# Performance work log

Measured on AMD Instinct MI355X. Metric: run time of the kernel, lower is better.

## Reference

```python
import jax, jax.numpy as jnp
import numpy as np

B, L, N, F = 8, 4096, 128, 128          # batch, pixels (64x64), memories, filters
H, DK, DV = 8, 16, 32                   # heads, key dim/head, value dim/head
TK, TV = H * DK, H * DV                 # total key depth 128, total value depth 256
BOT, FFN = 256, 2048                    # bottleneck (2*filters), feed-forward channels
EPS = 1e-3                              # keras BatchNormalization epsilon
INV = float(1.0 / np.sqrt(1.0 + EPS))   # inference BN with moving mean=0, var=1


def _bn_pair(k, shape):
    kg, kb = jax.random.split(k)
    gamma = jax.random.uniform(kg, shape, jnp.float32, 0.5, 1.5)
    beta = 0.1 * jax.random.normal(kb, shape, jnp.float32)
    return jnp.stack([gamma, beta])


def setup_inputs() -> dict:
    key = jax.random.key(0)
    ks = jax.random.split(key, 24)
    s = float(BOT) ** -0.5  # TruncatedNormal(stddev=bottleneck**-0.5) init for qkv convs
    return {
        "pixel_input": jax.random.normal(ks[0], (B, L, F), jnp.float32),
        "memory_input": jax.random.normal(ks[1], (B, N, F), jnp.float32),
        "W_mem1": 0.05 * jax.random.normal(ks[2], (F, BOT), jnp.float32),
        "bn_mem1": _bn_pair(ks[3], (BOT,)),
        "W_pix1": 0.05 * jax.random.normal(ks[4], (F, BOT), jnp.float32),
        "bn_pix1": _bn_pair(ks[5], (BOT,)),
        "W_mem_qkv": s * jax.random.normal(ks[6], (BOT, 2 * TK + TV), jnp.float32),
        "bn_mem_qkv": _bn_pair(ks[7], (2 * TK + TV,)),
        "W_pix_qkv": s * jax.random.normal(ks[8], (BOT, 2 * TK + TV), jnp.float32),
        "bn_pix_qkv": _bn_pair(ks[9], (2 * TK + TV,)),
        "bn_mem_sim": _bn_pair(ks[10], (H,)),
        "bn_mem_ret": _bn_pair(ks[11], (H, DV)),
        "bn_pix_sim": _bn_pair(ks[12], (H,)),
        "bn_pix_ret": _bn_pair(ks[13], (H, DV)),
        "W_mem3": 0.05 * jax.random.normal(ks[14], (TV, F), jnp.float32),
        "bn_mem3": _bn_pair(ks[15], (F,)),
        "W_pix3": 0.05 * jax.random.normal(ks[16], (TV, F), jnp.float32),
        "bn_pix3": _bn_pair(ks[17], (F,)),
        "W_ffn1": 0.05 * jax.random.normal(ks[18], (F, FFN), jnp.float32),
        "bn_ffn1": _bn_pair(ks[19], (FFN,)),
        "W_ffn2": 0.05 * jax.random.normal(ks[20], (FFN, F), jnp.float32),
        "bn_ffn2": _bn_pair(ks[21], (F,)),
    }


def _cbn(x, W, p, relu=False):
    """Conv1D (kernel=1) + inference BatchNorm over channels (+ optional relu)."""
    y = jnp.einsum('blc,cd->bld', x, W)
    y = y * (p[0] * INV) + p[1]
    return jax.nn.relu(y) if relu else y


def _heads(t, d):
    b, l, _ = t.shape  # [b, l, H*d] -> [b, H, l, d]
    return t.reshape(b, l, H, d).transpose(0, 2, 1, 3)


def reference(pixel_input, memory_input, W_mem1, bn_mem1, W_pix1, bn_pix1,
              W_mem_qkv, bn_mem_qkv, W_pix_qkv, bn_pix_qkv,
              bn_mem_sim, bn_mem_ret, bn_pix_sim, bn_pix_ret,
              W_mem3, bn_mem3, W_pix3, bn_pix3,
              W_ffn1, bn_ffn1, W_ffn2, bn_ffn2):
    # Bottleneck projections (conv1 + BN + relu)
    mem = _cbn(memory_input, W_mem1, bn_mem1, True)   # [B, N, BOT]
    pix = _cbn(pixel_input, W_pix1, bn_pix1, True)    # [B, L, BOT]

    # QKV projections (conv + BN, no activation)
    mqkv = _cbn(mem, W_mem_qkv, bn_mem_qkv)           # [B, N, 2*TK+TV]
    pqkv = _cbn(pix, W_pix_qkv, bn_pix_qkv)           # [B, L, 2*TK+TV]
    mq, mk, mv = mqkv[..., :TK], mqkv[..., TK:2 * TK], mqkv[..., 2 * TK:]
    pq, pk, pv = pqkv[..., :TK], pqkv[..., TK:2 * TK], pqkv[..., 2 * TK:]
    mq_h, mk_h = _heads(mq, DK), _heads(mk, DK)       # [B, H, N, DK]
    pq_h, pk_h = _heads(pq, DK), _heads(pk, DK)       # [B, H, L, DK]
    mv_h = mv.reshape(B, N, H, DV)                    # [B, N, H, DV]
    pv_h = pv.reshape(B, L, H, DV)                    # [B, L, H, DV]

    # Memory path: memory2pixel attention + memory self-attention share softmax
    k_cat = jnp.concatenate([pk_h, mk_h], axis=2)     # [B, H, L+N, DK]
    v_cat = jnp.concatenate([pv_h, mv_h], axis=1)     # [B, L+N, H, DV]
    logits = jnp.einsum('bhnd,bhmd->bhnm', mq_h, k_cat)
    logits = logits * (bn_mem_sim[0] * INV)[None, :, None, None] + bn_mem_sim[1][None, :, None, None]
    attn = jax.nn.softmax(logits, axis=-1)
    ret = jnp.einsum('bhnm,bmhd->bhnd', attn, v_cat)  # [B, H, N, DV]
    ret = ret * (bn_mem_ret[0] * INV)[None, :, None, :] + bn_mem_ret[1][None, :, None, :]
    ret = jax.nn.relu(ret).transpose(0, 2, 1, 3).reshape(B, N, TV)
    mem_out = jax.nn.relu(memory_input + _cbn(ret, W_mem3, bn_mem3))
    ffn = _cbn(mem_out, W_ffn1, bn_ffn1, True)
    mem_out = jax.nn.relu(mem_out + _cbn(ffn, W_ffn2, bn_ffn2))

    # Pixel path: pixel2memory feedback attention (sigmoid activation)
    plogits = jnp.einsum('bhld,bhnd->bhln', pq_h, mk_h)
    plogits = plogits * (bn_pix_sim[0] * INV)[None, :, None, None] + bn_pix_sim[1][None, :, None, None]
    pattn = jax.nn.sigmoid(plogits)
    pret = jnp.einsum('bhln,bnhd->bhld', pattn, mv_h)  # [B, H, L, DV]
    pret = pret * (bn_pix_ret[0] * INV)[None, :, None, :] + bn_pix_ret[1][None, :, None, :]
    pret = jax.nn.relu(pret).transpose(0, 2, 1, 3).reshape(B, L, TV)
    pix_out = jax.nn.relu(pixel_input + _cbn(pret, W_pix3, bn_pix3))

    return pix_out, mem_out
```

## Files before the change

kernel.cpp:

```cpp
#include <hip/hip_runtime.h>

typedef __attribute__((ext_vector_type(8))) short short8;
typedef __attribute__((ext_vector_type(4))) float floatx4;

#define INVC 0.9995003746877732f
#define NCHUNK 33

__device__ __forceinline__ unsigned short f2bf(float f) {
    union { float f; unsigned int u; } c; c.f = f;
    unsigned int r = c.u + 0x7fffu + ((c.u >> 16) & 1u);
    return (unsigned short)(r >> 16);
}
__device__ __forceinline__ unsigned int f2bf2(float a, float b) {
    return (unsigned int)f2bf(a) | ((unsigned int)f2bf(b) << 16);
}
__device__ __forceinline__ unsigned long long pack4(float v0, float v1, float v2, float v3) {
    return (unsigned long long)f2bf2(v0, v1) | ((unsigned long long)f2bf2(v2, v3) << 32);
}
__device__ __forceinline__ float bf2f(unsigned short u) {
    union { unsigned int u; float f; } c; c.u = ((unsigned int)u) << 16;
    return c.f;
}
__device__ __forceinline__ void gld_lds16(const unsigned short* g, unsigned short* l) {
    __builtin_amdgcn_global_load_lds(
        (const __attribute__((address_space(1))) unsigned int*)g,
        (__attribute__((address_space(3))) unsigned int*)l, 16, 0, 0);
}
__device__ __forceinline__ int fidx(int row, int k) {
    return (k >> 5) * 512 + (row + 16 * ((k >> 3) & 3)) * 8 + (k & 7);
}

struct PrepPtrs {
    const float* src_pix;
    unsigned short* dst_pix;
    const float* W[8]; unsigned short* Wt[8];
};

__global__ __launch_bounds__(256) void prep_kernel(PrepPtrs P) {
    __shared__ float T[32][33];
    const int bid = blockIdx.x, t = threadIdx.x;
    if (bid < 4096) {
        int i = bid * 1024 + t * 4;
        float4 v = *(const float4*)(P.src_pix + i);
        unsigned long long pk = pack4(v.x, v.y, v.z, v.w);
        *(unsigned long long*)(P.dst_pix + i) = pk;
        return;
    }
    int rel = bid - 4096;
    const int KD[8]  = {128,128,256,256,256,256,128,2048};
    const int ND[8]  = {256,256,512,512,128,128,2048,128};
    const int CNT[8] = {32,32,128,128,32,32,256,256};
    int wi = 0;
    #pragma unroll
    for (int k = 0; k < 8; ++k) { if (rel >= CNT[k] && wi == k) { rel -= CNT[k]; wi = k + 1; } }
    const int K = KD[wi], N = ND[wi];
    const int ntn = N >> 5;
    const int tn = rel % ntn, tk = rel / ntn;
    const int n0 = tn * 32, k0 = tk * 32;
    const float* W = P.W[wi];
    unsigned short* Wt = P.Wt[wi];
    const int tx = t & 31, ty = t >> 5;
    #pragma unroll
    for (int i = 0; i < 4; ++i)
        T[ty + 8*i][tx] = W[(size_t)(k0 + ty + 8*i) * N + n0 + tx];
    __syncthreads();
    #pragma unroll
    for (int i = 0; i < 4; ++i)
        Wt[(size_t)(n0 + ty + 8*i) * K + k0 + tx] = f2bf(T[tx][ty + 8*i]);
}

__device__ __forceinline__ void gemm_body(
    const unsigned short* __restrict__ A,
    const unsigned short* __restrict__ Bt,
    const float* __restrict__ bnp,
    const float* __restrict__ residF,
    float* __restrict__ outF,
    int K, int Nc, int row0, int col0,
    unsigned short* As, unsigned short* Bs)
{
    const int t = threadIdx.x;
    const int lane = t & 63, w = t >> 6;
    const int l15 = lane & 15, quad = lane >> 4;
    const int wr = w >> 1, wc = w & 1;

    floatx4 acc[4][4];
    #pragma unroll
    for (int i = 0; i < 4; ++i)
        #pragma unroll
        for (int j = 0; j < 4; ++j) acc[i][j] = (floatx4){0.f, 0.f, 0.f, 0.f};

    const unsigned short* gA0 = A  + (size_t)(row0 + w*16     + l15) * K + quad*8;
    const unsigned short* gA1 = A  + (size_t)(row0 + (w+4)*16 + l15) * K + quad*8;
    const unsigned short* gB0 = Bt + (size_t)(col0 + w*16     + l15) * K + quad*8;
    const unsigned short* gB1 = Bt + (size_t)(col0 + (w+4)*16 + l15) * K + quad*8;
    unsigned short* lA0 = &As[w * 512];
    unsigned short* lA1 = &As[(w + 4) * 512];
    unsigned short* lB0 = &Bs[w * 512];
    unsigned short* lB1 = &Bs[(w + 4) * 512];

    for (int k0 = 0; k0 < K; k0 += 32) {
        __syncthreads();
        gld_lds16(gA0 + k0, lA0);
        gld_lds16(gA1 + k0, lA1);
        gld_lds16(gB0 + k0, lB0);
        gld_lds16(gB1 + k0, lB1);
        __syncthreads();
        short8 a[4], b[4];
        #pragma unroll
        for (int mt = 0; mt < 4; ++mt) a[mt] = *(const short8*)&As[(wr*4 + mt)*512 + lane*8];
        #pragma unroll
        for (int nt = 0; nt < 4; ++nt) b[nt] = *(const short8*)&Bs[(wc*4 + nt)*512 + lane*8];
        #pragma unroll
        for (int mt = 0; mt < 4; ++mt)
            #pragma unroll
            for (int nt = 0; nt < 4; ++nt)
                acc[mt][nt] = __builtin_amdgcn_mfma_f32_16x16x32_bf16(a[mt], b[nt], acc[mt][nt], 0, 0, 0);
    }

    #pragma unroll
    for (int mt = 0; mt < 4; ++mt) {
        const int rowb = row0 + wr*64 + mt*16 + quad*4;
        #pragma unroll
        for (int nt = 0; nt < 4; ++nt) {
            const int col = col0 + wc*64 + nt*16 + l15;
            floatx4 v = acc[mt][nt];
            const float g  = bnp[col] * INVC;
            const float be = bnp[Nc + col];
            #pragma unroll
            for (int r = 0; r < 4; ++r) {
                size_t off = (size_t)(rowb + r) * Nc + col;
                float v1 = v[r] * g + be + residF[off];
                outF[off] = fmaxf(v1, 0.f);
            }
        }
    }
}

__global__ __launch_bounds__(256, 3) void k_qkv(
    const unsigned short* __restrict__ pixB,
    const unsigned short* __restrict__ Wt1, const float* __restrict__ bn1,
    const unsigned short* __restrict__ Wt2, const float* __restrict__ bnq,
    unsigned short* __restrict__ qip, unsigned short* __restrict__ kip,
    unsigned short* __restrict__ vtp,
    const float* __restrict__ memory_input,
    const unsigned short* __restrict__ Wm0, const float* __restrict__ bnm1,
    const unsigned short* __restrict__ Wm2, const float* __restrict__ bnmq,
    unsigned short* __restrict__ qim, unsigned short* __restrict__ kim,
    unsigned short* __restrict__ vtm)
{
    __shared__ unsigned short A2[32*512];
    const int t = threadIdx.x;
    const int lane = t & 63, w = t >> 6;
    const int l15 = lane & 15, quad = lane >> 4;

    if (blockIdx.x < 512) {
        const int row0 = blockIdx.x * 64;
        const int bb = row0 >> 12;
        const int runit0 = row0 >> 4;
        {
            short8 afr[4][4];
            float ga[4][4], ba[4][4];
            #pragma unroll
            for (int i = 0; i < 4; ++i) {
                #pragma unroll
                for (int kc = 0; kc < 4; ++kc)
                    afr[i][kc] = *(const short8*)&Wt1[(size_t)(w*64 + i*16 + l15)*128 + kc*32 + quad*8];
                #pragma unroll
                for (int r = 0; r < 4; ++r) {
                    const int col = w*64 + i*16 + quad*4 + r;
                    ga[i][r] = bn1[col] * INVC;
                    ba[i][r] = bn1[256 + col];
                }
            }
            #pragma unroll
            for (int ru = 0; ru < 4; ++ru) {
                short8 bfr[4];
                #pragma unroll
                for (int kc = 0; kc < 4; ++kc)
                    bfr[kc] = *(const short8*)&pixB[(size_t)(row0 + ru*16 + l15)*128 + kc*32 + quad*8];
                #pragma unroll
                for (int i = 0; i < 4; ++i) {
                    floatx4 acc = {0.f,0.f,0.f,0.f};
                    #pragma unroll
                    for (int kc = 0; kc < 4; ++kc)
                        acc = __builtin_amdgcn_mfma_f32_16x16x32_bf16(afr[i][kc], bfr[kc], acc, 0, 0, 0);
                    float v[4];
                    #pragma unroll
                    for (int r = 0; r < 4; ++r)
                        v[r] = fmaxf(acc[r]*ga[i][r] + ba[i][r], 0.f);
                    const int unit = ru*8 + w*2 + (i >> 1);
                    const int koff = (i & 1)*2 + (quad >> 1);
                    const int off  = unit*512 + (l15 + 16*koff)*8 + (quad & 1)*4;
                    uint2 pk; pk.x = f2bf2(v[0], v[1]); pk.y = f2bf2(v[2], v[3]);
                    *(uint2*)&A2[off] = pk;
                }
            }
        }
        __syncthreads();

        if (w < 2) {
            const int sec = w * 128;
            unsigned short* img = (w == 0) ? qip : kip;
            const int soff = (l15 + 16*(quad>>1))*8 + (quad&1)*4;
            for (int op = 0; op < 4; ++op) {
                short8 a0[8], a1[8];
                float g2[2][4], be2[2][4];
                #pragma unroll
                for (int kc = 0; kc < 8; ++kc) {
                    a0[kc] = *(const short8*)&Wt2[(size_t)(sec + (op*2+0)*16 + l15)*256 + kc*32 + quad*8];
                    a1[kc] = *(const short8*)&Wt2[(size_t)(sec + (op*2+1)*16 + l15)*256 + kc*32 + quad*8];
                }
                #pragma unroll
                for (int e = 0; e < 2; ++e)
                    #pragma unroll
                    for (int r = 0; r < 4; ++r) {
                        const int col = sec + (op*2+e)*16 + quad*4 + r;
                        g2[e][r] = bnq[col]*INVC; be2[e][r] = bnq[512+col];
                    }
                #pragma unroll
                for (int ru = 0; ru < 4; ++ru) {
                    short8 bv[8];
                    #pragma unroll
                    for (int kc = 0; kc < 8; ++kc)
                        bv[kc] = *(const short8*)&A2[(ru*8+kc)*512 + lane*8];
                    floatx4 acc0 = {0.f,0.f,0.f,0.f}, acc1 = {0.f,0.f,0.f,0.f};
                    #pragma unroll
                    for (int kc = 0; kc < 8; ++kc) {
                        acc0 = __builtin_amdgcn_mfma_f32_16x16x32_bf16(a0[kc], bv[kc], acc0, 0, 0, 0);
                        acc1 = __builtin_amdgcn_mfma_f32_16x16x32_bf16(a1[kc], bv[kc], acc1, 0, 0, 0);
                    }
                    unsigned long long pk0 = pack4(acc0[0]*g2[0][0]+be2[0][0], acc0[1]*g2[0][1]+be2[0][1],
                                                  acc0[2]*g2[0][2]+be2[0][2], acc0[3]*g2[0][3]+be2[0][3]);
                    unsigned long long pk1 = pack4(acc1[0]*g2[1][0]+be2[1][0], acc1[1]*g2[1][1]+be2[1][1],
                                                  acc1[2]*g2[1][2]+be2[1][2], acc1[3]*g2[1][3]+be2[1][3]);
                    *(unsigned long long*)&img[(size_t)((runit0+ru)*8 + op*2+0)*256 + soff] = pk0;
                    *(unsigned long long*)&img[(size_t)((runit0+ru)*8 + op*2+1)*256 + soff] = pk1;
                }
            }
        } else {
            const int dvb = (w-2)*128;
            for (int op = 0; op < 4; ++op) {
                short8 b0[8], b1[8];
                const int dvg0 = dvb + (op*2+0)*16 + l15;
                const int dvg1 = dvb + (op*2+1)*16 + l15;
                #pragma unroll
                for (int kc = 0; kc < 8; ++kc) {
                    b0[kc] = *(const short8*)&Wt2[(size_t)(256 + dvg0)*256 + kc*32 + quad*8];
                    b1[kc] = *(const short8*)&Wt2[(size_t)(256 + dvg1)*256 + kc*32 + quad*8];
                }
                const float gv0 = bnq[256 + dvg0]*INVC, bv0 = bnq[512 + 256 + dvg0];
                const float gv1 = bnq[256 + dvg1]*INVC, bv1 = bnq[512 + 256 + dvg1];
                const int h0 = dvg0 >> 5, dv16_0 = dvg0 & 15, du0 = (dvg0 >> 4) & 1;
                const int h1 = dvg1 >> 5, dv16_1 = dvg1 & 15, du1 = (dvg1 >> 4) & 1;
                #pragma unroll
                for (int ru = 0; ru < 4; ++ru) {
                    short8 av[8];
                    #pragma unroll
                    for (int kc = 0; kc < 8; ++kc)
                        av[kc] = *(const short8*)&A2[(ru*8+kc)*512 + lane*8];
                    floatx4 acc0 = {0.f,0.f,0.f,0.f}, acc1 = {0.f,0.f,0.f,0.f};
                    #pragma unroll
                    for (int kc = 0; kc < 8; ++kc) {
                        acc0 = __builtin_amdgcn_mfma_f32_16x16x32_bf16(av[kc], b0[kc], acc0, 0, 0, 0);
                        acc1 = __builtin_amdgcn_mfma_f32_16x16x32_bf16(av[kc], b1[kc], acc1, 0, 0, 0);
                    }
                    const int keyb = (row0 & 4095) + ru*16 + quad*4;
                    const int kcv = keyb >> 5;
                    const int g3 = (keyb >> 3) & 3;
                    const int jb = (quad & 1)*4;
                    unsigned long long pk0 = pack4(acc0[0]*gv0+bv0, acc0[1]*gv0+bv0,
                                                  acc0[2]*gv0+bv0, acc0[3]*gv0+bv0);
                    unsigned long long pk1 = pack4(acc1[0]*gv1+bv1, acc1[1]*gv1+bv1,
                                                  acc1[2]*gv1+bv1, acc1[3]*gv1+bv1);
                    size_t u0 = (size_t)((bb*8 + h0)*256 + (kcv>>2)*8 + du0*4 + (kcv&3))*512
                              + (dv16_0 + 16*g3)*8 + jb;
                    size_t u1 = (size_t)((bb*8 + h1)*256 + (kcv>>2)*8 + du1*4 + (kcv&3))*512
                              + (dv16_1 + 16*g3)*8 + jb;
                    *(unsigned long long*)&vtp[u0] = pk0;
                    *(unsigned long long*)&vtp[u1] = pk1;
                }
            }
        }
        return;
    }

    unsigned short* A0 = &A2[0];
    unsigned short* A1 = &A2[4*512];
    const int g0 = (blockIdx.x - 512) * 16;
    const int bb = g0 >> 7, ru = (g0 >> 4) & 7;
    {
        const int row = t >> 4;
        const int c0 = (t & 15) * 8;
        const float* src = memory_input + (size_t)(g0 + row) * 128 + c0;
        float4 v0 = *(const float4*)src;
        float4 v1 = *(const float4*)(src + 4);
        float vv[8] = {v0.x, v0.y, v0.z, v0.w, v1.x, v1.y, v1.z, v1.w};
        #pragma unroll
        for (int e = 0; e < 8; ++e)
            A0[fidx(row, c0 + e)] = f2bf(vv[e]);
    }
    __syncthreads();
    #pragma unroll
    for (int i = 0; i < 4; ++i) {
        const int n0 = (w*4 + i) * 16;
        floatx4 acc = {0.f,0.f,0.f,0.f};
        #pragma unroll
        for (int kc = 0; kc < 4; ++kc) {
            short8 a = *(const short8*)&A0[kc*512 + lane*8];
            short8 bfr = *(const short8*)&Wm0[(size_t)(n0 + l15)*128 + kc*32 + quad*8];
            acc = __builtin_amdgcn_mfma_f32_16x16x32_bf16(a, bfr, acc, 0, 0, 0);
        }
        const int col = n0 + l15;
        const float g = bnm1[col] * INVC, be = bnm1[256 + col];
        #pragma unroll
        for (int r = 0; r < 4; ++r)
            A1[fidx(quad*4 + r, col)] = f2bf(fmaxf(acc[r]*g + be, 0.f));
    }
    __syncthreads();
    if (w < 2) {
        const int sec = w * 128;
        unsigned short* img = (w == 0) ? qim : kim;
        const int soff = (l15 + 16*(quad>>1))*8 + (quad&1)*4;
        for (int op = 0; op < 4; ++op) {
            short8 a0[8], a1f[8];
            float g2[2][4], be2[2][4];
            #pragma unroll
            for (int kc = 0; kc < 8; ++kc) {
                a0[kc]  = *(const short8*)&Wm2[(size_t)(sec + (op*2+0)*16 + l15)*256 + kc*32 + quad*8];
                a1f[kc] = *(const short8*)&Wm2[(size_t)(sec + (op*2+1)*16 + l15)*256 + kc*32 + quad*8];
            }
            #pragma unroll
            for (int e = 0; e < 2; ++e)
                #pragma unroll
                for (int r = 0; r < 4; ++r) {
                    const int col = sec + (op*2+e)*16 + quad*4 + r;
                    g2[e][r] = bnmq[col]*INVC; be2[e][r] = bnmq[512+col];
                }
            short8 bv[8];
            #pragma unroll
            for (int kc = 0; kc < 8; ++kc)
                bv[kc] = *(const short8*)&A1[kc*512 + lane*8];
            floatx4 acc0 = {0.f,0.f,0.f,0.f}, acc1 = {0.f,0.f,0.f,0.f};
            #pragma unroll
            for (int kc = 0; kc < 8; ++kc) {
                acc0 = __builtin_amdgcn_mfma_f32_16x16x32_bf16(a0[kc],  bv[kc], acc0, 0, 0, 0);
                acc1 = __builtin_amdgcn_mfma_f32_16x16x32_bf16(a1f[kc], bv[kc], acc1, 0, 0, 0);
            }
            unsigned long long pk0 = pack4(acc0[0]*g2[0][0]+be2[0][0], acc0[1]*g2[0][1]+be2[0][1],
                                          acc0[2]*g2[0][2]+be2[0][2], acc0[3]*g2[0][3]+be2[0][3]);
            unsigned long long pk1 = pack4(acc1[0]*g2[1][0]+be2[1][0], acc1[1]*g2[1][1]+be2[1][1],
                                          acc1[2]*g2[1][2]+be2[1][2], acc1[3]*g2[1][3]+be2[1][3]);
            *(unsigned long long*)&img[(size_t)((bb*8+ru)*8 + op*2+0)*256 + soff] = pk0;
            *(unsigned long long*)&img[(size_t)((bb*8+ru)*8 + op*2+1)*256 + soff] = pk1;
        }
    } else {
        const int dvb = (w-2)*128;
        for (int op = 0; op < 4; ++op) {
            short8 b0[8], b1[8];
            const int dvg0 = dvb + (op*2+0)*16 + l15;
            const int dvg1 = dvb + (op*2+1)*16 + l15;
            #pragma unroll
            for (int kc = 0; kc < 8; ++kc) {
                b0[kc] = *(const short8*)&Wm2[(size_t)(256 + dvg0)*256 + kc*32 + quad*8];
                b1[kc] = *(const short8*)&Wm2[(size_t)(256 + dvg1)*256 + kc*32 + quad*8];
            }
            const float gv0 = bnmq[256 + dvg0]*INVC, bv0 = bnmq[512 + 256 + dvg0];
            const float gv1 = bnmq[256 + dvg1]*INVC, bv1 = bnmq[512 + 256 + dvg1];
            const int h0 = dvg0 >> 5, dv16_0 = dvg0 & 15, du0 = (dvg0 >> 4) & 1;
            const int h1 = dvg1 >> 5, dv16_1 = dvg1 & 15, du1 = (dvg1 >> 4) & 1;
            short8 av[8];
            #pragma unroll
            for (int kc = 0; kc < 8; ++kc)
                av[kc] = *(const short8*)&A1[kc*512 + lane*8];
            floatx4 acc0 = {0.f,0.f,0.f,0.f}, acc1 = {0.f,0.f,0.f,0.f};
            #pragma unroll
            for (int kc = 0; kc < 8; ++kc) {
                acc0 = __builtin_amdgcn_mfma_f32_16x16x32_bf16(av[kc], b0[kc], acc0, 0, 0, 0);
                acc1 = __builtin_amdgcn_mfma_f32_16x16x32_bf16(av[kc], b1[kc], acc1, 0, 0, 0);
            }
            const int keyb = (g0 & 127) + quad*4;
            const int kcv = keyb >> 5;
            const int g3 = (keyb >> 3) & 3;
            const int jb = (quad & 1)*4;
            unsigned long long pk0 = pack4(acc0[0]*gv0+bv0, acc0[1]*gv0+bv0,
                                          acc0[2]*gv0+bv0, acc0[3]*gv0+bv0);
            unsigned long long pk1 = pack4(acc1[0]*gv1+bv1, acc1[1]*gv1+bv1,
                                          acc1[2]*gv1+bv1, acc1[3]*gv1+bv1);
            size_t u0 = (size_t)((bb*8 + h0)*8 + du0*4 + kcv)*512 + (dv16_0 + 16*g3)*8 + jb;
            size_t u1 = (size_t)((bb*8 + h1)*8 + du1*4 + kcv)*512 + (dv16_1 + 16*g3)*8 + jb;
            *(unsigned long long*)&vtm[u0] = pk0;
            *(unsigned long long*)&vtm[u1] = pk1;
        }
    }
}

__global__ __launch_bounds__(256, 4) void k_attn(
    const unsigned short* __restrict__ qip, const unsigned short* __restrict__ kip,
    const unsigned short* __restrict__ vtp,
    const unsigned short* __restrict__ qim, const unsigned short* __restrict__ kim,
    const unsigned short* __restrict__ vtm,
    const float* __restrict__ bn_psim, const float* __restrict__ bn_pret,
    unsigned short* __restrict__ pret,
    const float* __restrict__ bn_msim,
    float* __restrict__ part_acc, float* __restrict__ part_ml)
{
    __shared__ unsigned short Qs[4*512];
    __shared__ unsigned short Ks[8*512];
    __shared__ unsigned short VsT[8*512];
    __shared__ unsigned short Ps[16*512];
    const int t = threadIdx.x;
    const int lane = t & 63, w = t >> 6;
    const int l15 = lane & 15, quad = lane >> 4;
    floatx4 z4 = {0.f, 0.f, 0.f, 0.f};

    const int is_pix = (blockIdx.x < 4096);
    int b, h, qrow0, c = 0, qh = 0;
    const unsigned short *qsrc, *ksrc0, *ksrc1, *vsrc0, *vsrc1;
    if (is_pix) {
        const int bx = blockIdx.x;
        const int lt = bx & 63; h = (bx >> 6) & 7; b = bx >> 9;
        qrow0 = b*4096 + lt*64;
        qsrc  = qip + (size_t)((b*256 + lt*4 + w)*8 + h)*256;
        ksrc0 = kim + (size_t)((b*8 + w)*8 + h)*256;
        ksrc1 = kim + (size_t)((b*8 + w+4)*8 + h)*256;
        vsrc0 = vtm + (size_t)((b*8+h)*8 + w)*512;
        vsrc1 = vtm + (size_t)((b*8+h)*8 + w+4)*512;
    } else {
        const int bxm = blockIdx.x - 4096;
        c = bxm % NCHUNK;
        const int rest = bxm / NCHUNK;
        qh = rest & 1; h = (rest >> 1) & 7; b = rest >> 4;
        qrow0 = b*128 + qh*64;
        qsrc = qim + (size_t)((b*8 + qh*4 + w)*8 + h)*256;
        if (c < 32) {
            ksrc0 = kip + (size_t)((b*256 + c*8 + w)*8 + h)*256;
            ksrc1 = kip + (size_t)((b*256 + c*8 + w+4)*8 + h)*256;
            vsrc0 = vtp + (size_t)((b*8+h)*256 + c*8 + w)*512;
            vsrc1 = vtp + (size_t)((b*8+h)*256 + c*8 + w+4)*512;
        } else {
            ksrc0 = kim + (size_t)((b*8 + w)*8 + h)*256;
            ksrc1 = kim + (size_t)((b*8 + w+4)*8 + h)*256;
            vsrc0 = vtm + (size_t)((b*8+h)*8 + w)*512;
            vsrc1 = vtm + (size_t)((b*8+h)*8 + w+4)*512;
        }
    }

    if (lane < 32) {
        gld_lds16(qsrc  + lane*8, &Qs[w*512]);
        gld_lds16(ksrc0 + lane*8, &Ks[w*512]);
        gld_lds16(ksrc1 + lane*8, &Ks[(w+4)*512]);
    }
    gld_lds16(vsrc0 + lane*8, &VsT[w*512]);
    gld_lds16(vsrc1 + lane*8, &VsT[(w+4)*512]);
    *(uint2*)&Qs[(t>>6)*512 + 256 + (t&63)*4] = make_uint2(0u, 0u);
    *(uint4*)&Ks[(t>>5)*512 + 256 + (t&31)*8] = make_uint4(0u,0u,0u,0u);
    __syncthreads();

    const float simg = (is_pix ? bn_psim[h] : bn_msim[h]) * INVC;
    const float simb =  is_pix ? bn_psim[8 + h] : bn_msim[8 + h];
    short8 bq = *(const short8*)&Qs[w*512 + lane*8];
    float mstat, lstat;

    if (is_pix) {
        #pragma unroll
        for (int nt = 0; nt < 8; ++nt) {
            short8 ak = *(const short8*)&Ks[nt*512 + lane*8];
            floatx4 s = __builtin_amdgcn_mfma_f32_16x16x32_bf16(ak, bq, z4, 0, 0, 0);
            float p[4];
            #pragma unroll
            for (int r = 0; r < 4; ++r) {
                float x = s[r] * simg + simb;
                p[r] = __builtin_amdgcn_rcpf(1.f + __expf(-x));
            }
            const int off = (w*4 + (nt>>1))*512
                          + (l15 + 16*((nt&1)*2 + (quad>>1)))*8 + (quad&1)*4;
            uint2 pk; pk.x = f2bf2(p[0], p[1]); pk.y = f2bf2(p[2], p[3]);
            *(uint2*)&Ps[off] = pk;
        }
    } else {
        floatx4 sv[8];
        float mx = -1e30f;
        #pragma unroll
        for (int nt = 0; nt < 8; ++nt) {
            short8 ak = *(const short8*)&Ks[nt*512 + lane*8];
            floatx4 s = __builtin_amdgcn_mfma_f32_16x16x32_bf16(ak, bq, z4, 0, 0, 0);
            #pragma unroll
            for (int r = 0; r < 4; ++r) {
                sv[nt][r] = s[r] * simg + simb;
                mx = fmaxf(mx, sv[nt][r]);
            }
        }
        mx = fmaxf(mx, __shfl_xor(mx, 16));
        mx = fmaxf(mx, __shfl_xor(mx, 32));
        float lsum = 0.f;
        #pragma unroll
        for (int nt = 0; nt < 8; ++nt) {
            float p[4];
            #pragma unroll
            for (int r = 0; r < 4; ++r) {
                p[r] = __expf(sv[nt][r] - mx);
                lsum += p[r];
            }
            const int off = (w*4 + (nt>>1))*512
                          + (l15 + 16*((nt&1)*2 + (quad>>1)))*8 + (quad&1)*4;
            uint2 pk; pk.x = f2bf2(p[0], p[1]); pk.y = f2bf2(p[2], p[3]);
            *(uint2*)&Ps[off] = pk;
        }
        lsum += __shfl_xor(lsum, 16);
        lsum += __shfl_xor(lsum, 32);
        mstat = mx; lstat = lsum;
    }

    #pragma unroll
    for (int dvt = 0; dvt < 2; ++dvt) {
        floatx4 acc = {0.f,0.f,0.f,0.f};
        #pragma unroll
        for (int ks = 0; ks < 4; ++ks) {
            short8 av = *(const short8*)&VsT[(dvt*4 + ks)*512 + lane*8];
            short8 bp = *(const short8*)&Ps[(w*4 + ks)*512 + lane*8];
            acc = __builtin_amdgcn_mfma_f32_16x16x32_bf16(av, bp, acc, 0, 0, 0);
        }
        if (is_pix) {
            const int q = qrow0 + w*16 + l15;
            float v[4];
            #pragma unroll
            for (int r = 0; r < 4; ++r) {
                const int dv = dvt*16 + quad*4 + r;
                v[r] = fmaxf(acc[r] * (bn_pret[h*32 + dv]*INVC) + bn_pret[256 + h*32 + dv], 0.f);
            }
            *(unsigned long long*)&pret[((size_t)q << 8) + h*32 + dvt*16 + quad*4]
                = pack4(v[0], v[1], v[2], v[3]);
        } else {
            const int bh = b*8 + h;
            const int q = qh*64 + w*16 + l15;
            float4 st = make_float4(acc[0], acc[1], acc[2], acc[3]);
            *(float4*)&part_acc[((size_t)(bh*NCHUNK + c)*128 + q)*32 + dvt*16 + quad*4] = st;
        }
    }
    if (!is_pix && quad == 0) {
        const int bh = b*8 + h;
        const int q = qh*64 + w*16 + l15;
        size_t o = ((size_t)(bh*NCHUNK + c)*128 + q) * 2;
        *(float2*)&part_ml[o] = make_float2(mstat, lstat);
    }
}

__global__ __launch_bounds__(256) void k_pix3_combmem3(
    const unsigned short* __restrict__ pretB, const unsigned short* __restrict__ Wt5,
    const float* __restrict__ bn_pix3, const float* __restrict__ pixel_input,
    float* __restrict__ out_pix,
    const float* __restrict__ part_acc, const float* __restrict__ part_ml,
    const float* __restrict__ bn_ret,
    const unsigned short* __restrict__ Wt4, const float* __restrict__ bn3,
    const float* __restrict__ memory_input,
    unsigned short* __restrict__ moB)
{
    __shared__ unsigned short As[8 * 512];
    __shared__ unsigned short Bs[8 * 512];
    const int bx = blockIdx.x;
    if (bx < 256) {
        gemm_body(pretB, Wt5, bn_pix3, pixel_input, out_pix, 256, 128,
                  bx * 128, 0, As, Bs);
        return;
    }
    unsigned short* mretA = As;
    const int t = threadIdx.x;
    const int lane = t & 63, w = t >> 6;
    const int l15 = lane & 15, quad = lane >> 4;
    const int g0 = (bx - 256) * 16;
    const int b = g0 >> 7;
    const int nbase = g0 & 127;

    {
        const int row = t >> 4;
        const int c0 = (t & 15) * 16;
        const int h = c0 >> 5;
        const int n = nbase + row;
        const int bh = b*8 + h;
        float m_g = -1e30f;
        for (int s = 0; s < NCHUNK; ++s)
            m_g = fmaxf(m_g, part_ml[((size_t)(bh*NCHUNK + s)*128 + n)*2]);
        float l_g = 0.f;
        float og[16];
        #pragma unroll
        for (int e = 0; e < 16; ++e) og[e] = 0.f;
        for (int s = 0; s < NCHUNK; ++s) {
            size_t o = ((size_t)(bh*NCHUNK + s)*128 + n)*2;
            float wgt = __expf(part_ml[o] - m_g);
            l_g += part_ml[o+1] * wgt;
            const float* pa = part_acc + ((size_t)(bh*NCHUNK + s)*128 + n)*32 + (c0 & 31);
            #pragma unroll
            for (int e = 0; e < 16; e += 4) {
                float4 v = *(const float4*)(pa + e);
                og[e]   += v.x*wgt; og[e+1] += v.y*wgt;
                og[e+2] += v.z*wgt; og[e+3] += v.w*wgt;
            }
        }
        float invl = __builtin_amdgcn_rcpf(l_g);
        #pragma unroll
        for (int e = 0; e < 16; ++e) {
            int col = c0 + e;
            int dv = col & 31;
            float v = og[e]*invl*(bn_ret[h*32+dv]*INVC) + bn_ret[256 + h*32 + dv];
            mretA[fidx(row, col)] = f2bf(fmaxf(v, 0.f));
        }
    }
    __syncthreads();

    #pragma unroll
    for (int i = 0; i < 2; ++i) {
        const int n0 = (w*2 + i) * 16;
        floatx4 acc = {0.f,0.f,0.f,0.f};
        #pragma unroll
        for (int kc = 0; kc < 8; ++kc) {
            short8 a = *(const short8*)&mretA[kc*512 + lane*8];
            short8 bfr = *(const short8*)&Wt4[(size_t)(n0 + l15)*256 + kc*32 + quad*8];
            acc = __builtin_amdgcn_mfma_f32_16x16x32_bf16(a, bfr, acc, 0, 0, 0);
        }
        const int col = n0 + l15;
        const float g = bn3[col]*INVC, be = bn3[128 + col];
        #pragma unroll
        for (int r = 0; r < 4; ++r) {
            const int row = quad*4 + r;
            float v = acc[r]*g + be + memory_input[(size_t)(g0 + row)*128 + col];
            moB[(size_t)(g0 + row)*128 + col] = f2bf(fmaxf(v, 0.f));
        }
    }
}

__global__ __launch_bounds__(1024) void k_ffn(
    const unsigned short* __restrict__ moB,
    const unsigned short* __restrict__ Wt6, const float* __restrict__ bnf1,
    const unsigned short* __restrict__ Wt7, const float* __restrict__ bnf2,
    float* __restrict__ out_mem)
{
    __shared__ unsigned short moA[4*512];
    __shared__ unsigned short fA[64*512];
    __shared__ floatx4 red[2][8][64];
    const int t = threadIdx.x;
    const int lane = t & 63, w = t >> 6;
    const int l15 = lane & 15, quad = lane >> 4;
    const int g0 = blockIdx.x * 16;

    if (t < 256) {
        const int row = t >> 4;
        const int c0 = (t & 15) * 8;
        uint4 v = *(const uint4*)(moB + (size_t)(g0 + row)*128 + c0);
        unsigned short ev[8] = {
            (unsigned short)(v.x & 0xffffu), (unsigned short)(v.x >> 16),
            (unsigned short)(v.y & 0xffffu), (unsigned short)(v.y >> 16),
            (unsigned short)(v.z & 0xffffu), (unsigned short)(v.z >> 16),
            (unsigned short)(v.w & 0xffffu), (unsigned short)(v.w >> 16)};
        #pragma unroll
        for (int e = 0; e < 8; ++e) moA[fidx(row, c0+e)] = ev[e];
    }
    __syncthreads();

    #pragma unroll
    for (int i = 0; i < 8; ++i) {
        const int n0 = (w*8 + i) * 16;
        floatx4 acc = {0.f,0.f,0.f,0.f};
        #pragma unroll
        for (int kc = 0; kc < 4; ++kc) {
            short8 a = *(const short8*)&moA[kc*512 + lane*8];
            short8 bfr = *(const short8*)&Wt6[(size_t)(n0 + l15)*128 + kc*32 + quad*8];
            acc = __builtin_amdgcn_mfma_f32_16x16x32_bf16(a, bfr, acc, 0, 0, 0);
        }
        const int col = n0 + l15;
        const float g = bnf1[col]*INVC, be = bnf1[2048 + col];
        #pragma unroll
        for (int r = 0; r < 4; ++r)
            fA[fidx(quad*4 + r, col)] = f2bf(fmaxf(acc[r]*g + be, 0.f));
    }
    __syncthreads();

    {
        const int ntile = w & 7, khalf = w >> 3;
        const int n0 = ntile * 16;
        floatx4 acc = {0.f,0.f,0.f,0.f};
        #pragma unroll 8
        for (int kc = 0; kc < 32; ++kc) {
            const int kcu = khalf*32 + kc;
            short8 a = *(const short8*)&fA[kcu*512 + lane*8];
            short8 bfr = *(const short8*)&Wt7[(size_t)(n0 + l15)*2048 + kcu*32 + quad*8];
            acc = __builtin_amdgcn_mfma_f32_16x16x32_bf16(a, bfr, acc, 0, 0, 0);
        }
        red[khalf][ntile][lane] = acc;
    }
    __syncthreads();
    if (w < 8) {
        const int n0 = w * 16;
        floatx4 s0 = red[0][w][lane];
        floatx4 s1 = red[1][w][lane];
        const int col = n0 + l15;
        const float g = bnf2[col]*INVC, be = bnf2[128 + col];
        #pragma unroll
        for (int r = 0; r < 4; ++r) {
            const int row = quad*4 + r;
            float resid = bf2f(moA[fidx(row, col)]);
            float v = fmaxf((s0[r] + s1[r])*g + be + resid, 0.f);
            out_mem[(size_t)(g0 + row)*128 + col] = v;
        }
    }
}

extern "C" void kernel_launch(void* const* d_in, const int* in_sizes, int n_in,
                              void* d_out, int out_size, void* d_ws, size_t ws_size,
                              hipStream_t stream) {
    const float* pixel_input  = (const float*)d_in[0];
    const float* memory_input = (const float*)d_in[1];
    const float* W_mem1    = (const float*)d_in[2];
    const float* bn_mem1   = (const float*)d_in[3];
    const float* W_pix1    = (const float*)d_in[4];
    const float* bn_pix1   = (const float*)d_in[5];
    const float* W_mem_qkv = (const float*)d_in[6];
    const float* bn_mem_qkv= (const float*)d_in[7];
    const float* W_pix_qkv = (const float*)d_in[8];
    const float* bn_pix_qkv= (const float*)d_in[9];
    const float* bn_mem_sim= (const float*)d_in[10];
    const float* bn_mem_ret= (const float*)d_in[11];
    const float* bn_pix_sim= (const float*)d_in[12];
    const float* bn_pix_ret= (const float*)d_in[13];
    const float* W_mem3    = (const float*)d_in[14];
    const float* bn_mem3   = (const float*)d_in[15];
    const float* W_pix3    = (const float*)d_in[16];
    const float* bn_pix3   = (const float*)d_in[17];
    const float* W_ffn1    = (const float*)d_in[18];
    const float* bn_ffn1   = (const float*)d_in[19];
    const float* W_ffn2    = (const float*)d_in[20];
    const float* bn_ffn2   = (const float*)d_in[21];

    char* ws = (char*)d_ws;
    size_t off = 0;
    auto alloc = [&](size_t bytes) -> void* {
        void* p = ws + off; off += (bytes + 255) & ~(size_t)255; return p;
    };
    unsigned short* pixB  = (unsigned short*)alloc((size_t)32768*128*2);
    unsigned short* Wt0   = (unsigned short*)alloc((size_t)256*128*2);
    unsigned short* Wt1   = (unsigned short*)alloc((size_t)256*128*2);
    unsigned short* Wt2   = (unsigned short*)alloc((size_t)512*256*2);
    unsigned short* Wt3   = (unsigned short*)alloc((size_t)512*256*2);
    unsigned short* Wt4   = (unsigned short*)alloc((size_t)128*256*2);
    unsigned short* Wt5   = (unsigned short*)alloc((size_t)128*256*2);
    unsigned short* Wt6   = (unsigned short*)alloc((size_t)2048*128*2);
    unsigned short* Wt7   = (unsigned short*)alloc((size_t)128*2048*2);
    unsigned short* qip   = (unsigned short*)alloc((size_t)2048*8*256*2);
    unsigned short* kip   = (unsigned short*)alloc((size_t)2048*8*256*2);
    unsigned short* vtp   = (unsigned short*)alloc((size_t)64*256*512*2);
    unsigned short* qim   = (unsigned short*)alloc((size_t)64*8*256*2);
    unsigned short* kim   = (unsigned short*)alloc((size_t)64*8*256*2);
    unsigned short* vtm   = (unsigned short*)alloc((size_t)64*8*512*2);
    float* part_acc = (float*)alloc((size_t)64*NCHUNK*128*32*4);
    float* part_ml  = (float*)alloc((size_t)64*NCHUNK*128*2*4);
    unsigned short* pretB = (unsigned short*)alloc((size_t)32768*256*2);
    unsigned short* moB   = (unsigned short*)alloc((size_t)1024*128*2);

    float* out_pix = (float*)d_out;
    float* out_mem = (float*)d_out + (size_t)8*4096*128;

    PrepPtrs P;
    P.src_pix = pixel_input;
    P.dst_pix = pixB;
    P.W[0]=W_mem1; P.W[1]=W_pix1; P.W[2]=W_mem_qkv; P.W[3]=W_pix_qkv;
    P.W[4]=W_mem3; P.W[5]=W_pix3; P.W[6]=W_ffn1;    P.W[7]=W_ffn2;
    P.Wt[0]=Wt0; P.Wt[1]=Wt1; P.Wt[2]=Wt2; P.Wt[3]=Wt3;
    P.Wt[4]=Wt4; P.Wt[5]=Wt5; P.Wt[6]=Wt6; P.Wt[7]=Wt7;

    dim3 blk(256);
    prep_kernel<<<4992, blk, 0, stream>>>(P);
    k_qkv<<<576, blk, 0, stream>>>(pixB, Wt1, bn_pix1, Wt3, bn_pix_qkv,
        qip, kip, vtp,
        memory_input, Wt0, bn_mem1, Wt2, bn_mem_qkv, qim, kim, vtm);
    k_attn<<<4096 + 128*NCHUNK, blk, 0, stream>>>(qip, kip, vtp, qim, kim, vtm,
        bn_pix_sim, bn_pix_ret, pretB, bn_mem_sim, part_acc, part_ml);
    k_pix3_combmem3<<<320, blk, 0, stream>>>(pretB, Wt5, bn_pix3, pixel_input, out_pix,
        part_acc, part_ml, bn_mem_ret, Wt4, bn_mem3, memory_input, moB);
    k_ffn<<<64, dim3(1024), 0, stream>>>(moB, Wt6, bn_ffn1, Wt7, bn_ffn2, out_mem);
}
```

Before: 238.7 us.

## Replace split-KV memory attention with in-block online softmax; bf16 pixel residual

```diff
diff --git a/kernel.cpp b/kernel.cpp
--- a/kernel.cpp
+++ b/kernel.cpp
@@ -4,7 +4,6 @@
 typedef __attribute__((ext_vector_type(4))) float floatx4;
 
 #define INVC 0.9995003746877732f
-#define NCHUNK 33
 
 __device__ __forceinline__ unsigned short f2bf(float f) {
     union { float f; unsigned int u; } c; c.f = f;
@@ -73,7 +72,7 @@
     const unsigned short* __restrict__ A,
     const unsigned short* __restrict__ Bt,
     const float* __restrict__ bnp,
-    const float* __restrict__ residF,
+    const unsigned short* __restrict__ residB,
     float* __restrict__ outF,
     int K, int Nc, int row0, int col0,
     unsigned short* As, unsigned short* Bs)
@@ -129,7 +128,7 @@
             #pragma unroll
             for (int r = 0; r < 4; ++r) {
                 size_t off = (size_t)(rowb + r) * Nc + col;
-                float v1 = v[r] * g + be + residF[off];
+                float v1 = v[r] * g + be + bf2f(residB[off]);
                 outF[off] = fmaxf(v1, 0.f);
             }
         }
@@ -401,8 +400,8 @@
     const unsigned short* __restrict__ vtm,
     const float* __restrict__ bn_psim, const float* __restrict__ bn_pret,
     unsigned short* __restrict__ pret,
-    const float* __restrict__ bn_msim,
-    float* __restrict__ part_acc, float* __restrict__ part_ml)
+    const float* __restrict__ bn_msim, const float* __restrict__ bn_mret,
+    unsigned short* __restrict__ mretF)
 {
     __shared__ unsigned short Qs[4*512];
     __shared__ unsigned short Ks[8*512];
@@ -413,55 +412,31 @@
     const int l15 = lane & 15, quad = lane >> 4;
     floatx4 z4 = {0.f, 0.f, 0.f, 0.f};
 
-    const int is_pix = (blockIdx.x < 4096);
-    int b, h, qrow0, c = 0, qh = 0;
-    const unsigned short *qsrc, *ksrc0, *ksrc1, *vsrc0, *vsrc1;
-    if (is_pix) {
+    if (blockIdx.x < 4096) {
         const int bx = blockIdx.x;
-        const int lt = bx & 63; h = (bx >> 6) & 7; b = bx >> 9;
-        qrow0 = b*4096 + lt*64;
-        qsrc  = qip + (size_t)((b*256 + lt*4 + w)*8 + h)*256;
-        ksrc0 = kim + (size_t)((b*8 + w)*8 + h)*256;
-        ksrc1 = kim + (size_t)((b*8 + w+4)*8 + h)*256;
-        vsrc0 = vtm + (size_t)((b*8+h)*8 + w)*512;
-        vsrc1 = vtm + (size_t)((b*8+h)*8 + w+4)*512;
-    } else {
-        const int bxm = blockIdx.x - 4096;
-        c = bxm % NCHUNK;
-        const int rest = bxm / NCHUNK;
-        qh = rest & 1; h = (rest >> 1) & 7; b = rest >> 4;
-        qrow0 = b*128 + qh*64;
-        qsrc = qim + (size_t)((b*8 + qh*4 + w)*8 + h)*256;
-        if (c < 32) {
-            ksrc0 = kip + (size_t)((b*256 + c*8 + w)*8 + h)*256;
-            ksrc1 = kip + (size_t)((b*256 + c*8 + w+4)*8 + h)*256;
-            vsrc0 = vtp + (size_t)((b*8+h)*256 + c*8 + w)*512;
-            vsrc1 = vtp + (size_t)((b*8+h)*256 + c*8 + w+4)*512;
-        } else {
-            ksrc0 = kim + (size_t)((b*8 + w)*8 + h)*256;
-            ksrc1 = kim + (size_t)((b*8 + w+4)*8 + h)*256;
-            vsrc0 = vtm + (size_t)((b*8+h)*8 + w)*512;
-            vsrc1 = vtm + (size_t)((b*8+h)*8 + w+4)*512;
-        }
-    }
-
-    if (lane < 32) {
-        gld_lds16(qsrc  + lane*8, &Qs[w*512]);
-        gld_lds16(ksrc0 + lane*8, &Ks[w*512]);
-        gld_lds16(ksrc1 + lane*8, &Ks[(w+4)*512]);
-    }
-    gld_lds16(vsrc0 + lane*8, &VsT[w*512]);
-    gld_lds16(vsrc1 + lane*8, &VsT[(w+4)*512]);
-    *(uint2*)&Qs[(t>>6)*512 + 256 + (t&63)*4] = make_uint2(0u, 0u);
-    *(uint4*)&Ks[(t>>5)*512 + 256 + (t&31)*8] = make_uint4(0u,0u,0u,0u);
-    __syncthreads();
-
-    const float simg = (is_pix ? bn_psim[h] : bn_msim[h]) * INVC;
-    const float simb =  is_pix ? bn_psim[8 + h] : bn_msim[8 + h];
-    short8 bq = *(const short8*)&Qs[w*512 + lane*8];
-    float mstat, lstat;
-
-    if (is_pix) {
+        const int lt = bx & 63; const int h = (bx >> 6) & 7; const int b = bx >> 9;
+        const int qrow0 = b*4096 + lt*64;
+        const unsigned short* qsrc  = qip + (size_t)((b*256 + lt*4 + w)*8 + h)*256;
+        const unsigned short* ksrc0 = kim + (size_t)((b*8 + w)*8 + h)*256;
+        const unsigned short* ksrc1 = kim + (size_t)((b*8 + w+4)*8 + h)*256;
+        const unsigned short* vsrc0 = vtm + (size_t)((b*8+h)*8 + w)*512;
+        const unsigned short* vsrc1 = vtm + (size_t)((b*8+h)*8 + w+4)*512;
+
+        if (lane < 32) {
+            gld_lds16(qsrc  + lane*8, &Qs[w*512]);
+            gld_lds16(ksrc0 + lane*8, &Ks[w*512]);
+            gld_lds16(ksrc1 + lane*8, &Ks[(w+4)*512]);
+        }
+        gld_lds16(vsrc0 + lane*8, &VsT[w*512]);
+        gld_lds16(vsrc1 + lane*8, &VsT[(w+4)*512]);
+        *(uint2*)&Qs[(t>>6)*512 + 256 + (t&63)*4] = make_uint2(0u, 0u);
+        *(uint4*)&Ks[(t>>5)*512 + 256 + (t&31)*8] = make_uint4(0u,0u,0u,0u);
+        __syncthreads();
+
+        const float simg = bn_psim[h] * INVC;
+        const float simb = bn_psim[8 + h];
+        short8 bq = *(const short8*)&Qs[w*512 + lane*8];
+
         #pragma unroll
         for (int nt = 0; nt < 8; ++nt) {
             short8 ak = *(const short8*)&Ks[nt*512 + lane*8];
@@ -477,7 +452,68 @@
             uint2 pk; pk.x = f2bf2(p[0], p[1]); pk.y = f2bf2(p[2], p[3]);
             *(uint2*)&Ps[off] = pk;
         }
-    } else {
+
+        #pragma unroll
+        for (int dvt = 0; dvt < 2; ++dvt) {
+            floatx4 acc = {0.f,0.f,0.f,0.f};
+            #pragma unroll
+            for (int ks = 0; ks < 4; ++ks) {
+                short8 av = *(const short8*)&VsT[(dvt*4 + ks)*512 + lane*8];
+                short8 bp = *(const short8*)&Ps[(w*4 + ks)*512 + lane*8];
+                acc = __builtin_amdgcn_mfma_f32_16x16x32_bf16(av, bp, acc, 0, 0, 0);
+            }
+            const int q = qrow0 + w*16 + l15;
+            float v[4];
+            #pragma unroll
+            for (int r = 0; r < 4; ++r) {
+                const int dv = dvt*16 + quad*4 + r;
+                v[r] = fmaxf(acc[r] * (bn_pret[h*32 + dv]*INVC) + bn_pret[256 + h*32 + dv], 0.f);
+            }
+            *(unsigned long long*)&pret[((size_t)q << 8) + h*32 + dvt*16 + quad*4]
+                = pack4(v[0], v[1], v[2], v[3]);
+        }
+        return;
+    }
+
+    const int bxm = blockIdx.x - 4096;
+    const int qh = bxm & 1; const int h = (bxm >> 1) & 7; const int b = bxm >> 4;
+    const unsigned short* qsrc = qim + (size_t)((b*8 + qh*4 + w)*8 + h)*256;
+    if (lane < 32) gld_lds16(qsrc + lane*8, &Qs[w*512]);
+    *(uint2*)&Qs[(t>>6)*512 + 256 + (t&63)*4] = make_uint2(0u, 0u);
+    *(uint4*)&Ks[(t>>5)*512 + 256 + (t&31)*8] = make_uint4(0u,0u,0u,0u);
+    __syncthreads();
+
+    const float simg = bn_msim[h] * INVC;
+    const float simb = bn_msim[8 + h];
+    short8 bq = *(const short8*)&Qs[w*512 + lane*8];
+
+    float m_run = -1e30f, l_run = 0.f;
+    floatx4 accpv[2];
+    accpv[0] = (floatx4){0.f,0.f,0.f,0.f};
+    accpv[1] = (floatx4){0.f,0.f,0.f,0.f};
+
+    for (int c = 0; c < 33; ++c) {
+        __syncthreads();
+        const unsigned short *ks0, *ks1, *vs0, *vs1;
+        if (c < 32) {
+            ks0 = kip + (size_t)((b*256 + c*8 + w)*8 + h)*256;
+            ks1 = kip + (size_t)((b*256 + c*8 + w+4)*8 + h)*256;
+            vs0 = vtp + (size_t)((b*8+h)*256 + c*8 + w)*512;
+            vs1 = vtp + (size_t)((b*8+h)*256 + c*8 + w+4)*512;
+        } else {
+            ks0 = kim + (size_t)((b*8 + w)*8 + h)*256;
+            ks1 = kim + (size_t)((b*8 + w+4)*8 + h)*256;
+            vs0 = vtm + (size_t)((b*8+h)*8 + w)*512;
+            vs1 = vtm + (size_t)((b*8+h)*8 + w+4)*512;
+        }
+        if (lane < 32) {
+            gld_lds16(ks0 + lane*8, &Ks[w*512]);
+            gld_lds16(ks1 + lane*8, &Ks[(w+4)*512]);
+        }
+        gld_lds16(vs0 + lane*8, &VsT[w*512]);
+        gld_lds16(vs1 + lane*8, &VsT[(w+4)*512]);
+        __syncthreads();
+
         floatx4 sv[8];
         float mx = -1e30f;
         #pragma unroll
@@ -492,13 +528,15 @@
         }
         mx = fmaxf(mx, __shfl_xor(mx, 16));
         mx = fmaxf(mx, __shfl_xor(mx, 32));
+        float newm = fmaxf(m_run, mx);
+        float alpha = __expf(m_run - newm);
         float lsum = 0.f;
         #pragma unroll
         for (int nt = 0; nt < 8; ++nt) {
             float p[4];
             #pragma unroll
             for (int r = 0; r < 4; ++r) {
-                p[r] = __expf(sv[nt][r] - mx);
+                p[r] = __expf(sv[nt][r] - newm);
                 lsum += p[r];
             }
             const int off = (w*4 + (nt>>1))*512
@@ -508,49 +546,45 @@
         }
         lsum += __shfl_xor(lsum, 16);
         lsum += __shfl_xor(lsum, 32);
-        mstat = mx; lstat = lsum;
-    }
-
+        l_run = l_run * alpha + lsum;
+        m_run = newm;
+        accpv[0] *= alpha;
+        accpv[1] *= alpha;
+
+        #pragma unroll
+        for (int dvt = 0; dvt < 2; ++dvt) {
+            floatx4 a = accpv[dvt];
+            #pragma unroll
+            for (int ks = 0; ks < 4; ++ks) {
+                short8 av = *(const short8*)&VsT[(dvt*4 + ks)*512 + lane*8];
+                short8 bp = *(const short8*)&Ps[(w*4 + ks)*512 + lane*8];
+                a = __builtin_amdgcn_mfma_f32_16x16x32_bf16(av, bp, a, 0, 0, 0);
+            }
+            accpv[dvt] = a;
+        }
+    }
+
+    const float invl = __builtin_amdgcn_rcpf(l_run);
+    const int qunit = b*8 + qh*4 + w;
     #pragma unroll
     for (int dvt = 0; dvt < 2; ++dvt) {
-        floatx4 acc = {0.f,0.f,0.f,0.f};
-        #pragma unroll
-        for (int ks = 0; ks < 4; ++ks) {
-            short8 av = *(const short8*)&VsT[(dvt*4 + ks)*512 + lane*8];
-            short8 bp = *(const short8*)&Ps[(w*4 + ks)*512 + lane*8];
-            acc = __builtin_amdgcn_mfma_f32_16x16x32_bf16(av, bp, acc, 0, 0, 0);
-        }
-        if (is_pix) {
-            const int q = qrow0 + w*16 + l15;
-            float v[4];
-            #pragma unroll
-            for (int r = 0; r < 4; ++r) {
-                const int dv = dvt*16 + quad*4 + r;
-                v[r] = fmaxf(acc[r] * (bn_pret[h*32 + dv]*INVC) + bn_pret[256 + h*32 + dv], 0.f);
-            }
-            *(unsigned long long*)&pret[((size_t)q << 8) + h*32 + dvt*16 + quad*4]
-                = pack4(v[0], v[1], v[2], v[3]);
-        } else {
-            const int bh = b*8 + h;
-            const int q = qh*64 + w*16 + l15;
-            float4 st = make_float4(acc[0], acc[1], acc[2], acc[3]);
-            *(float4*)&part_acc[((size_t)(bh*NCHUNK + c)*128 + q)*32 + dvt*16 + quad*4] = st;
-        }
-    }
-    if (!is_pix && quad == 0) {
-        const int bh = b*8 + h;
-        const int q = qh*64 + w*16 + l15;
-        size_t o = ((size_t)(bh*NCHUNK + c)*128 + q) * 2;
-        *(float2*)&part_ml[o] = make_float2(mstat, lstat);
+        float v[4];
+        #pragma unroll
+        for (int r = 0; r < 4; ++r) {
+            const int dv = dvt*16 + quad*4 + r;
+            v[r] = fmaxf(accpv[dvt][r]*invl*(bn_mret[h*32 + dv]*INVC) + bn_mret[256 + h*32 + dv], 0.f);
+        }
+        size_t off = (size_t)(qunit*8 + h)*512
+                   + (l15 + 16*(dvt*2 + (quad>>1)))*8 + (quad&1)*4;
+        *(unsigned long long*)&mretF[off] = pack4(v[0], v[1], v[2], v[3]);
     }
 }
 
 __global__ __launch_bounds__(256) void k_pix3_combmem3(
     const unsigned short* __restrict__ pretB, const unsigned short* __restrict__ Wt5,
-    const float* __restrict__ bn_pix3, const float* __restrict__ pixel_input,
+    const float* __restrict__ bn_pix3, const unsigned short* __restrict__ pixB,
     float* __restrict__ out_pix,
-    const float* __restrict__ part_acc, const float* __restrict__ part_ml,
-    const float* __restrict__ bn_ret,
+    const unsigned short* __restrict__ mretF,
     const unsigned short* __restrict__ Wt4, const float* __restrict__ bn3,
     const float* __restrict__ memory_input,
     unsigned short* __restrict__ moB)
@@ -559,7 +593,7 @@
     __shared__ unsigned short Bs[8 * 512];
     const int bx = blockIdx.x;
     if (bx < 256) {
-        gemm_body(pretB, Wt5, bn_pix3, pixel_input, out_pix, 256, 128,
+        gemm_body(pretB, Wt5, bn_pix3, pixB, out_pix, 256, 128,
                   bx * 128, 0, As, Bs);
         return;
     }
@@ -568,43 +602,10 @@
     const int lane = t & 63, w = t >> 6;
     const int l15 = lane & 15, quad = lane >> 4;
     const int g0 = (bx - 256) * 16;
-    const int b = g0 >> 7;
-    const int nbase = g0 & 127;
-
-    {
-        const int row = t >> 4;
-        const int c0 = (t & 15) * 16;
-        const int h = c0 >> 5;
-        const int n = nbase + row;
-        const int bh = b*8 + h;
-        float m_g = -1e30f;
-        for (int s = 0; s < NCHUNK; ++s)
-            m_g = fmaxf(m_g, part_ml[((size_t)(bh*NCHUNK + s)*128 + n)*2]);
-        float l_g = 0.f;
-        float og[16];
-        #pragma unroll
-        for (int e = 0; e < 16; ++e) og[e] = 0.f;
-        for (int s = 0; s < NCHUNK; ++s) {
-            size_t o = ((size_t)(bh*NCHUNK + s)*128 + n)*2;
-            float wgt = __expf(part_ml[o] - m_g);
-            l_g += part_ml[o+1] * wgt;
-            const float* pa = part_acc + ((size_t)(bh*NCHUNK + s)*128 + n)*32 + (c0 & 31);
-            #pragma unroll
-            for (int e = 0; e < 16; e += 4) {
-                float4 v = *(const float4*)(pa + e);
-                og[e]   += v.x*wgt; og[e+1] += v.y*wgt;
-                og[e+2] += v.z*wgt; og[e+3] += v.w*wgt;
-            }
-        }
-        float invl = __builtin_amdgcn_rcpf(l_g);
-        #pragma unroll
-        for (int e = 0; e < 16; ++e) {
-            int col = c0 + e;
-            int dv = col & 31;
-            float v = og[e]*invl*(bn_ret[h*32+dv]*INVC) + bn_ret[256 + h*32 + dv];
-            mretA[fidx(row, col)] = f2bf(fmaxf(v, 0.f));
-        }
-    }
+    const int qunit = g0 >> 4;
+
+    gld_lds16(mretF + (size_t)(qunit*8 + w)*512 + lane*8, &mretA[w*512]);
+    gld_lds16(mretF + (size_t)(qunit*8 + w+4)*512 + lane*8, &mretA[(w+4)*512]);
     __syncthreads();
 
     #pragma unroll
@@ -750,8 +751,7 @@
     unsigned short* qim   = (unsigned short*)alloc((size_t)64*8*256*2);
     unsigned short* kim   = (unsigned short*)alloc((size_t)64*8*256*2);
     unsigned short* vtm   = (unsigned short*)alloc((size_t)64*8*512*2);
-    float* part_acc = (float*)alloc((size_t)64*NCHUNK*128*32*4);
-    float* part_ml  = (float*)alloc((size_t)64*NCHUNK*128*2*4);
+    unsigned short* mretF = (unsigned short*)alloc((size_t)64*8*512*2);
     unsigned short* pretB = (unsigned short*)alloc((size_t)32768*256*2);
     unsigned short* moB   = (unsigned short*)alloc((size_t)1024*128*2);
 
@@ -771,9 +771,9 @@
     k_qkv<<<576, blk, 0, stream>>>(pixB, Wt1, bn_pix1, Wt3, bn_pix_qkv,
         qip, kip, vtp,
         memory_input, Wt0, bn_mem1, Wt2, bn_mem_qkv, qim, kim, vtm);
-    k_attn<<<4096 + 128*NCHUNK, blk, 0, stream>>>(qip, kip, vtp, qim, kim, vtm,
-        bn_pix_sim, bn_pix_ret, pretB, bn_mem_sim, part_acc, part_ml);
-    k_pix3_combmem3<<<320, blk, 0, stream>>>(pretB, Wt5, bn_pix3, pixel_input, out_pix,
-        part_acc, part_ml, bn_mem_ret, Wt4, bn_mem3, memory_input, moB);
+    k_attn<<<4096 + 128, blk, 0, stream>>>(qip, kip, vtp, qim, kim, vtm,
+        bn_pix_sim, bn_pix_ret, pretB, bn_mem_sim, bn_mem_ret, mretF);
+    k_pix3_combmem3<<<320, blk, 0, stream>>>(pretB, Wt5, bn_pix3, pixB, out_pix,
+        mretF, Wt4, bn_mem3, memory_input, moB);
     k_ffn<<<64, dim3(1024), 0, stream>>>(moB, Wt6, bn_ffn1, Wt7, bn_ffn2, out_mem);
 }
```

Result: slower. 259.8 us (+8.8%).
